# Kernel tuning notes

Measured on AMD Instinct MI355X. Metric: run time of the kernel, lower is better.

Reference implementation:

```python
import jax, jax.numpy as jnp
import numpy as np

E = 8          # num_experts
T = 16384      # total tokens (sum of expert_size)
D = 1024       # d_model
F = 4096       # d_ff


def setup_inputs() -> dict:
    key = jax.random.key(0)
    k_x, k_w1, k_w2 = jax.random.split(key, 3)
    s1 = 1.0 / np.sqrt(D)
    s2 = 1.0 / np.sqrt(F)
    return {
        "inputs": jax.random.normal(k_x, (T, D), dtype=jnp.float32),
        # equal-sized per-expert chunks (reference assumes uniform routing)
        "expert_size": jnp.full((E,), T // E, dtype=jnp.int32),
        "w1": jax.random.normal(k_w1, (E, D, F), dtype=jnp.float32) * s1,
        "b1": jnp.zeros((E, F), dtype=jnp.float32),
        "w2": jax.random.normal(k_w2, (E, F, D), dtype=jnp.float32) * s2,
        "b2": jnp.zeros((E, D), dtype=jnp.float32),
    }


def reference(inputs, expert_size, w1, b1, w2, b2):
    """ParallelExperts forward: split tokens by expert_size, run each expert
    (Linear->GELU->Linear), concat. With equal chunk sizes the split+loop+concat
    is exactly a grouped (batched-per-expert) GEMM, expressed here as one
    reshape + batched einsum instead of a Python loop of small matmuls."""
    e = w1.shape[0]
    t, d = inputs.shape
    x = inputs.reshape(e, t // e, d)                      # [E, T/E, D]
    h = jax.nn.gelu(jnp.einsum('etd,edf->etf', x, w1) + b1[:, None, :])
    y = jnp.einsum('etf,efd->etd', h, w2) + b2[:, None, :]
    return y.reshape(t, d)
```

## Files before the change

kernel.cpp:

```cpp
#include <hip/hip_runtime.h>

typedef unsigned short ushort_t;
typedef __attribute__((ext_vector_type(8))) unsigned short ushortx8;
typedef __attribute__((ext_vector_type(8))) __bf16 bf16x8;
typedef __attribute__((ext_vector_type(4))) float floatx4;

#define NE 8
#define NT 16384
#define ND 1024
#define NF 4096
#define MPE (NT / NE)

__device__ __forceinline__ float b2f(ushort_t x) {
    unsigned u = ((unsigned)x) << 16;
    float f;
    __builtin_memcpy(&f, &u, 4);
    return f;
}
__device__ __forceinline__ ushort_t f2b(float f) {
    unsigned u;
    __builtin_memcpy(&u, &f, 4);
    u += 0x7FFFu + ((u >> 16) & 1u);
    return (ushort_t)(u >> 16);
}
__device__ __forceinline__ float gelu_tanh(float x) {
    float u = x + 0.044715f * x * x * x;
    float e = __expf(1.5957691216f * u);
    float t = 1.0f - 2.0f / (e + 1.0f);
    return 0.5f * x * (1.0f + t);
}

__global__ void detect_dtype(const ushort_t* __restrict__ x, int* __restrict__ flag) {
    int l = threadIdx.x;
    float v = b2f(x[2 * l]);
    float a = fabsf(v);
    int big = (a > 1e4f) || (a != a);
    unsigned long long m = __ballot(big);
    if (l == 0) *flag = (__popcll(m) >= 4) ? 1 : 0;
}

__global__ __launch_bounds__(256) void conv_bf16(
    const void* __restrict__ src, ushort_t* __restrict__ dst, int n,
    const int* __restrict__ flagp)
{
    int flag = *flagp;
    int i = (blockIdx.x * 256 + threadIdx.x) * 8;
    if (i >= n) return;
    if (flag) {
        const float* s = (const float*)src + i;
        ushortx8 o;
#pragma unroll
        for (int j = 0; j < 8; ++j) o[j] = f2b(s[j]);
        *(ushortx8*)(dst + i) = o;
    } else {
        *(ushortx8*)(dst + i) = *(const ushortx8*)((const ushort_t*)src + i);
    }
}

__global__ __launch_bounds__(256) void transpose_e(
    const void* __restrict__ src, ushort_t* __restrict__ dst, int R, int C,
    const int* __restrict__ flagp)
{
    __shared__ __align__(16) ushort_t tile[64 * 64];
    int flag = *flagp;
    int e = blockIdx.z;
    size_t ebase = (size_t)e * R * C;
    int r0 = blockIdx.y * 64, c0 = blockIdx.x * 64;
    int t = threadIdx.x;
#pragma unroll
    for (int i = 0; i < 2; ++i) {
        int ch = t + 256 * i;
        int r  = ch >> 3;
        int c8 = ch & 7;
        size_t gi = ebase + (size_t)(r0 + r) * C + (c0 + c8 * 8);
        ushortx8 v;
        if (flag) {
            const float* s = (const float*)src + gi;
#pragma unroll
            for (int j = 0; j < 8; ++j) v[j] = f2b(s[j]);
        } else {
            v = *(const ushortx8*)((const ushort_t*)src + gi);
        }
        *(ushortx8*)&tile[r * 64 + ((c8 ^ ((r >> 3) & 7)) * 8)] = v;
    }
    __syncthreads();
#pragma unroll
    for (int i = 0; i < 2; ++i) {
        int ch  = t + 256 * i;
        int oc  = ch >> 3;
        int orr = (ch & 7) * 8;
        ushortx8 v;
#pragma unroll
        for (int j = 0; j < 8; ++j) {
            int rr = orr + j;
            v[j] = tile[rr * 64 + (((oc >> 3) ^ ((rr >> 3) & 7)) * 8) + (oc & 7)];
        }
        *(ushortx8*)(dst + ebase + (size_t)(c0 + oc) * R + (r0 + orr)) = v;
    }
}

template <int GELU, int DUALOUT>
__global__ __launch_bounds__(512, 2) void gemm_bt8(
    const ushort_t* __restrict__ A, const ushort_t* __restrict__ Bt,
    const ushort_t* __restrict__ bias, void* __restrict__ Cout,
    int Mpe, int N, int K, const int* __restrict__ flagp)
{
    __shared__ __align__(16) ushort_t sA[2][256 * 64];
    __shared__ __align__(16) ushort_t sB[2][256 * 64];

    const int flag = DUALOUT ? *flagp : 0;
    const int e  = blockIdx.z;
    const int m0 = blockIdx.y * 256;
    const int n0 = blockIdx.x * 256;
    const ushort_t* Ae = A  + (size_t)e * Mpe * K + (size_t)m0 * K;
    const ushort_t* Be = Bt + (size_t)e * N   * K + (size_t)n0 * K;

    const int t  = threadIdx.x;
    const int w  = t >> 6;
    const int l  = t & 63;
    const int wr = w >> 2;
    const int wc = w & 3;
    const int lwr = l >> 3;
    const int swz = (l & 7) ^ lwr;
    const int q  = l >> 4;
    const int ln = l & 15;

    const int KT = K >> 6;

#define STAGE(G, S, r0c, kcol) do {                                          \
        int rb_ = (r0c) + w * 8;                                             \
        const ushort_t* ga_ = (G) + (size_t)(rb_ + lwr) * K + (kcol) + swz * 8; \
        __builtin_amdgcn_global_load_lds(                                    \
            (const __attribute__((address_space(1))) void*)ga_,              \
            (__attribute__((address_space(3))) void*)&(S)[rb_ * 64], 16, 0, 0); \
    } while (0)

    floatx4 acc[8][4] = {};

    STAGE(Ae, sA[0],   0, 0); STAGE(Ae, sA[0],  64, 0);
    STAGE(Ae, sA[0], 128, 0); STAGE(Ae, sA[0], 192, 0);
    STAGE(Be, sB[0],   0, 0); STAGE(Be, sB[0],  64, 0);
    STAGE(Be, sB[0], 128, 0); STAGE(Be, sB[0], 192, 0);
    if (KT > 1) {
        STAGE(Ae, sA[1],   0, 64);
        STAGE(Ae, sA[1], 128, 64);
        asm volatile("s_waitcnt vmcnt(2)" ::: "memory");
    } else {
        asm volatile("s_waitcnt vmcnt(0)" ::: "memory");
    }
    __builtin_amdgcn_s_barrier();

    for (int kt = 0; kt < KT; ++kt) {
        const int cur = kt & 1;
        ushort_t* sAc = &sA[cur][0];
        ushort_t* sBc = &sB[cur][0];
        ushort_t* sAn = &sA[cur ^ 1][0];
        ushort_t* sBn = &sB[cur ^ 1][0];
        const int kc = kt * 64;

#pragma unroll
        for (int p = 0; p < 4; ++p) {
            const int qm = p >> 1, qn = p & 1;

            bf16x8 af[2][4], bv[2][2];
#pragma unroll
            for (int ks = 0; ks < 2; ++ks) {
#pragma unroll
                for (int mi = 0; mi < 4; ++mi) {
                    int m = wr * 128 + qm * 64 + mi * 16 + ln;
                    af[ks][mi] = *(const bf16x8*)&sAc[m * 64 + (((ks * 4 + q) ^ (m & 7)) * 8)];
                }
#pragma unroll
                for (int nj = 0; nj < 2; ++nj) {
                    int n = wc * 64 + qn * 32 + nj * 16 + ln;
                    bv[ks][nj] = *(const bf16x8*)&sBc[n * 64 + (((ks * 4 + q) ^ (n & 7)) * 8)];
                }
            }

            if (p == 0 && kt + 1 < KT) {
                STAGE(Ae, sAn,  64, kc + 64);
                STAGE(Ae, sAn, 192, kc + 64);
                STAGE(Be, sBn,   0, kc + 64);
                STAGE(Be, sBn,  64, kc + 64);
            }
            if (p == 1 && kt + 1 < KT) {
                STAGE(Be, sBn, 128, kc + 64);
                STAGE(Be, sBn, 192, kc + 64);
            }
            if (p == 2 && kt + 2 < KT) {
                STAGE(Ae, sAc,   0, kc + 128);
                STAGE(Ae, sAc, 128, kc + 128);
            }

            __builtin_amdgcn_s_barrier();
            asm volatile("s_waitcnt lgkmcnt(0)" ::: "memory");
            __builtin_amdgcn_sched_barrier(0);

            __builtin_amdgcn_s_setprio(1);
#pragma unroll
            for (int ks = 0; ks < 2; ++ks)
#pragma unroll
                for (int mi = 0; mi < 4; ++mi)
#pragma unroll
                    for (int nj = 0; nj < 2; ++nj)
                        acc[qm * 4 + mi][qn * 2 + nj] =
                            __builtin_amdgcn_mfma_f32_16x16x32_bf16(
                                af[ks][mi], bv[ks][nj],
                                acc[qm * 4 + mi][qn * 2 + nj], 0, 0, 0);
            __builtin_amdgcn_s_setprio(0);

            if (p == 3) {
                if (kt + 2 < KT) asm volatile("s_waitcnt vmcnt(2)" ::: "memory");
                else             asm volatile("s_waitcnt vmcnt(0)" ::: "memory");
            }
            __builtin_amdgcn_s_barrier();
        }
    }
#undef STAGE

    const ushort_t* be = bias + (size_t)e * N + n0;
#pragma unroll
    for (int qn = 0; qn < 2; ++qn) {
#pragma unroll
        for (int nj = 0; nj < 2; ++nj) {
            int col = wc * 64 + qn * 32 + nj * 16 + ln;
            float bvv = b2f(be[col]);
#pragma unroll
            for (int qm = 0; qm < 2; ++qm) {
#pragma unroll
                for (int mi = 0; mi < 4; ++mi) {
#pragma unroll
                    for (int r = 0; r < 4; ++r) {
                        int row = wr * 128 + qm * 64 + mi * 16 + q * 4 + r;
                        float v = acc[qm * 4 + mi][qn * 2 + nj][r] + bvv;
                        if (GELU) v = gelu_tanh(v);
                        size_t idx = (size_t)e * Mpe * N + (size_t)(m0 + row) * N + (n0 + col);
                        if (DUALOUT && flag) ((float*)Cout)[idx] = v;
                        else                 ((ushort_t*)Cout)[idx] = f2b(v);
                    }
                }
            }
        }
    }
}

extern "C" void kernel_launch(void* const* d_in, const int* in_sizes, int n_in,
                              void* d_out, int out_size, void* d_ws, size_t ws_size,
                              hipStream_t stream) {
    const void* x  = d_in[0];
    const void* w1 = d_in[2];
    const void* b1 = d_in[3];
    const void* w2 = d_in[4];
    const void* b2 = d_in[5];

    char* ws = (char*)d_ws;
    int*      flag = (int*)ws;
    ushort_t* xb   = (ushort_t*)(ws + ((size_t)1  << 20));
    ushort_t* b1b  = (ushort_t*)(ws + ((size_t)34 << 20));
    ushort_t* b2b  = (ushort_t*)(ws + ((size_t)35 << 20));
    ushort_t* wT   = (ushort_t*)(ws + ((size_t)36 << 20));
    ushort_t* H    = (ushort_t*)(ws + ((size_t)100 << 20));

    detect_dtype<<<1, 64, 0, stream>>>((const ushort_t*)x, flag);

    conv_bf16<<<(NT * ND / 8 + 255) / 256, 256, 0, stream>>>(x,  xb,  NT * ND, flag);
    conv_bf16<<<(NE * NF / 8 + 255) / 256, 256, 0, stream>>>(b1, b1b, NE * NF, flag);
    conv_bf16<<<(NE * ND / 8 + 255) / 256, 256, 0, stream>>>(b2, b2b, NE * ND, flag);

    transpose_e<<<dim3(NF / 64, ND / 64, NE), 256, 0, stream>>>(w1, wT, ND, NF, flag);
    gemm_bt8<1, 0><<<dim3(NF / 256, MPE / 256, NE), 512, 0, stream>>>(
        xb, wT, b1b, H, MPE, NF, ND, flag);
    transpose_e<<<dim3(ND / 64, NF / 64, NE), 256, 0, stream>>>(w2, wT, NF, ND, flag);
    gemm_bt8<0, 1><<<dim3(ND / 256, MPE / 256, NE), 512, 0, stream>>>(
        H, wT, b2b, d_out, MPE, ND, NF, flag);
}
```

Baseline: 767.0 us.

## Add double-buffered LDS-direct GEMM with XCD swizzle for second expert GEMM

Adds a new gemm_g2 kernel used only for the second grouped GEMM (H x W2). It stages tiles straight into two LDS buffers with global_load_lds, so the load for the next K tile is issued before the MFMAs on the current one. It also remaps block IDs so consecutive tiles land on the same XCD for better L2 reuse. In exchange it uses 128KB of LDS per block with launch_bounds(512,2), which may limit occupancy, and the swizzle assumes power-of-two grid dimensions.

```diff
diff --git a/kernel.cpp b/kernel.cpp
--- a/kernel.cpp
+++ b/kernel.cpp
@@ -244,6 +244,152 @@
     }
 }
 
+template <int GELU, int DUALOUT>
+__global__ __launch_bounds__(512, 2) void gemm_g2(
+    const ushort_t* __restrict__ A, const ushort_t* __restrict__ Bt,
+    const ushort_t* __restrict__ bias, void* __restrict__ Cout,
+    int Mpe, int N, int K, const int* __restrict__ flagp)
+{
+    __shared__ __align__(16) ushort_t sA[2][256 * 64];
+    __shared__ __align__(16) ushort_t sB[2][256 * 64];
+
+    const int flag = DUALOUT ? *flagp : 0;
+
+    const unsigned gx = gridDim.x, gy = gridDim.y;
+    unsigned bid = blockIdx.x + gx * (blockIdx.y + gy * blockIdx.z);
+    unsigned nwg = gx * gy * gridDim.z;
+    unsigned cpx = nwg >> 3;
+    unsigned sw  = (bid & 7) * cpx + (bid >> 3);
+    unsigned lx = __ffs(gx) - 1, ly = __ffs(gy) - 1;
+    const int e  = sw >> (lx + ly);
+    const int m0 = ((sw >> lx) & (gy - 1)) * 256;
+    const int n0 = (sw & (gx - 1)) * 256;
+
+    const ushort_t* Ae = A  + (size_t)e * Mpe * K + (size_t)m0 * K;
+    const ushort_t* Be = Bt + (size_t)e * N   * K + (size_t)n0 * K;
+
+    const int t  = threadIdx.x;
+    const int w  = t >> 6;
+    const int l  = t & 63;
+    const int wr = w >> 2;
+    const int wc = w & 3;
+    const int lwr = l >> 3;
+    const int swz = (l & 7) ^ lwr;
+    const int q  = l >> 4;
+    const int ln = l & 15;
+
+    const int KT = K >> 6;
+
+#define STAGE(G, S, r0c, kcol) do {                                          \
+        int rb_ = (r0c) + w * 8;                                             \
+        const ushort_t* ga_ = (G) + (size_t)(rb_ + lwr) * K + (kcol) + swz * 8; \
+        __builtin_amdgcn_global_load_lds(                                    \
+            (const __attribute__((address_space(1))) void*)ga_,              \
+            (__attribute__((address_space(3))) void*)&(S)[rb_ * 64], 16, 0, 0); \
+    } while (0)
+
+#define STAGE8(AT, BT, kcol) do {                                            \
+        STAGE(Ae, AT,   0, kcol); STAGE(Ae, AT,  64, kcol);                  \
+        STAGE(Ae, AT, 128, kcol); STAGE(Ae, AT, 192, kcol);                  \
+        STAGE(Be, BT,   0, kcol); STAGE(Be, BT,  64, kcol);                  \
+        STAGE(Be, BT, 128, kcol); STAGE(Be, BT, 192, kcol);                  \
+    } while (0)
+
+    floatx4 acc[8][4] = {};
+
+#define KSTEP(SAc, SBc, SAn, SBn, kcn, PRE) do {                             \
+        if (PRE) { STAGE8(SAn, SBn, kcn); }                                  \
+        bf16x8 a0[2][4], a1[2][4], b0[2][2], b1[2][2];                       \
+        _Pragma("unroll")                                                    \
+        for (int ks = 0; ks < 2; ++ks) {                                     \
+            _Pragma("unroll")                                                \
+            for (int mi = 0; mi < 4; ++mi) {                                 \
+                int m  = wr * 128 + mi * 16 + ln;                            \
+                int m2 = m + 64;                                             \
+                a0[ks][mi] = *(const bf16x8*)&(SAc)[m  * 64 + (((ks * 4 + q) ^ (m  & 7)) * 8)]; \
+                a1[ks][mi] = *(const bf16x8*)&(SAc)[m2 * 64 + (((ks * 4 + q) ^ (m2 & 7)) * 8)]; \
+            }                                                                \
+            _Pragma("unroll")                                                \
+            for (int nj = 0; nj < 2; ++nj) {                                 \
+                int n  = wc * 64 + nj * 16 + ln;                             \
+                int n2 = n + 32;                                             \
+                b0[ks][nj] = *(const bf16x8*)&(SBc)[n  * 64 + (((ks * 4 + q) ^ (n  & 7)) * 8)]; \
+                b1[ks][nj] = *(const bf16x8*)&(SBc)[n2 * 64 + (((ks * 4 + q) ^ (n2 & 7)) * 8)]; \
+            }                                                                \
+        }                                                                    \
+        _Pragma("unroll")                                                    \
+        for (int ks = 0; ks < 2; ++ks)                               \
+            _Pragma("unroll")                                                \
+            for (int mi = 0; mi < 4; ++mi)                                   \
+                _Pragma("unroll")                                            \
+                for (int nj = 0; nj < 2; ++nj)                               \
+                    acc[mi][nj] = __builtin_amdgcn_mfma_f32_16x16x32_bf16(   \
+                        a0[ks][mi], b0[ks][nj], acc[mi][nj], 0, 0, 0);       \
+        _Pragma("unroll")                                                    \
+        for (int ks = 0; ks < 2; ++ks)                               \
+            _Pragma("unroll")                                                \
+            for (int mi = 0; mi < 4; ++mi)                                   \
+                _Pragma("unroll")                                            \
+                for (int nj = 0; nj < 2; ++nj)                               \
+                    acc[mi][2 + nj] = __builtin_amdgcn_mfma_f32_16x16x32_bf16( \
+                        a0[ks][mi], b1[ks][nj], acc[mi][2 + nj], 0, 0, 0);   \
+        _Pragma("unroll")                                                    \
+        for (int ks = 0; ks < 2; ++ks)                               \
+            _Pragma("unroll")                                                \
+            for (int mi = 0; mi < 4; ++mi)                                   \
+                _Pragma("unroll")                                            \
+                for (int nj = 0; nj < 2; ++nj)                               \
+                    acc[4 + mi][2 + nj] = __builtin_amdgcn_mfma_f32_16x16x32_bf16( \
+                        a1[ks][mi], b1[ks][nj], acc[4 + mi][2 + nj], 0, 0, 0); \
+        _Pragma("unroll")                                                    \
+        for (int ks = 0; ks < 2; ++ks)                               \
+            _Pragma("unroll")                                                \
+            for (int mi = 0; mi < 4; ++mi)                                   \
+                _Pragma("unroll")                                            \
+                for (int nj = 0; nj < 2; ++nj)                               \
+                    acc[4 + mi][nj] = __builtin_amdgcn_mfma_f32_16x16x32_bf16( \
+                        a1[ks][mi], b0[ks][nj], acc[4 + mi][nj], 0, 0, 0);   \
+        __syncthreads();                                                     \
+    } while (0)
+
+    STAGE8(sA[0], sB[0], 0);
+    __syncthreads();
+
+    for (int kt = 0; kt < KT; kt += 2) {
+        const int kc = kt * 64;
+        KSTEP(sA[0], sB[0], sA[1], sB[1], kc + 64,  true);
+        KSTEP(sA[1], sB[1], sA[0], sB[0], kc + 128, (kt + 2 < KT));
+    }
+#undef KSTEP
+#undef STAGE8
+#undef STAGE
+
+    const ushort_t* be = bias + (size_t)e * N + n0;
+#pragma unroll
+    for (int qn = 0; qn < 2; ++qn) {
+#pragma unroll
+        for (int nj = 0; nj < 2; ++nj) {
+            int col = wc * 64 + qn * 32 + nj * 16 + ln;
+            float bvv = b2f(be[col]);
+#pragma unroll
+            for (int qm = 0; qm < 2; ++qm) {
+#pragma unroll
+                for (int mi = 0; mi < 4; ++mi) {
+#pragma unroll
+                    for (int r = 0; r < 4; ++r) {
+                        int row = wr * 128 + qm * 64 + mi * 16 + q * 4 + r;
+                        float v = acc[qm * 4 + mi][qn * 2 + nj][r] + bvv;
+                        if (GELU) v = gelu_tanh(v);
+                        size_t idx = (size_t)e * Mpe * N + (size_t)(m0 + row) * N + (n0 + col);
+                        if (DUALOUT && flag) ((float*)Cout)[idx] = v;
+                        else                 ((ushort_t*)Cout)[idx] = f2b(v);
+                    }
+                }
+            }
+        }
+    }
+}
+
 extern "C" void kernel_launch(void* const* d_in, const int* in_sizes, int n_in,
                               void* d_out, int out_size, void* d_ws, size_t ws_size,
                               hipStream_t stream) {
@@ -271,6 +417,6 @@
     gemm_bt8<1, 0><<<dim3(NF / 256, MPE / 256, NE), 512, 0, stream>>>(
         xb, wT, b1b, H, MPE, NF, ND, flag);
     transpose_e<<<dim3(ND / 64, NF / 64, NE), 256, 0, stream>>>(w2, wT, NF, ND, flag);
-    gemm_bt8<0, 1><<<dim3(ND / 256, MPE / 256, NE), 512, 0, stream>>>(
+    gemm_g2<0, 1><<<dim3(ND / 256, MPE / 256, NE), 512, 0, stream>>>(
         H, wT, b2b, d_out, MPE, ND, NF, flag);
 }
```

New measurement: 743.4 us. 1.03x faster.
